# Kernel optimization log

Hardware: AMD Instinct MI355X
Metric: run time of the kernel (lower is better)

The kernel has to match this reference:

```python
import jax, jax.numpy as jnp
import numpy as np

# irreps layout: 256x0e (dim 256) + 128x1o (dim 384) + 64x2e (dim 320) -> total 960
MULS = (256, 128, 64)
DIMS = (1, 3, 5)  # 2l+1 for l = 0, 1, 2


def setup_inputs() -> dict:
    key = jax.random.key(0)
    k0, k1, k2, k3 = jax.random.split(key, 4)
    N = 131072
    total = sum(m * d for m, d in zip(MULS, DIMS))  # 960
    return {
        "features": jax.random.normal(k0, (N, total), dtype=jnp.float32),
        "w0": jax.random.normal(k1, (256, 256), dtype=jnp.float32),
        "w1": jax.random.normal(k2, (128, 128), dtype=jnp.float32),
        "w2": jax.random.normal(k3, (64, 64), dtype=jnp.float32),
    }


def _linear_irreps(features, weights):
    # Equivariant Linear == block-diagonal per-irrep matmul over the multiplicity
    # axis, broadcast over the (2l+1) m-components, scaled by 1/sqrt(mul_in)
    # (the net of e3nn's path_weight sqrt((2l+1)/mul_in) and the w3j 1/sqrt(2l+1)).
    outs = []
    off = 0
    for w, mul, d in zip(weights, MULS, DIMS):
        x = features[:, off:off + mul * d].reshape(-1, mul, d)  # [N, u, i]
        scale = 1.0 / np.sqrt(mul).astype(np.float32)
        y = jnp.einsum('zui,uw->zwi', x, w) * scale  # [N, w, i]
        outs.append(y.reshape(y.shape[0], mul * d))
        off += mul * d
    return jnp.concatenate(outs, axis=-1)  # [N, 960]


def reference(features, w0, w1, w2):
    return _linear_irreps(features, (w0, w1, w2))
```

## Files before the change

### kernel.cpp

```cpp
#include <hip/hip_runtime.h>

typedef short bf16x8 __attribute__((ext_vector_type(8)));
typedef float f32x4 __attribute__((ext_vector_type(4)));

__device__ __forceinline__ unsigned short f2bf(float f) {
    union { float f; unsigned u; } a; a.f = f;
    unsigned u = a.u;
    u += 0x7fffu + ((u >> 16) & 1u);
    return (unsigned short)(u >> 16);
}

__device__ __forceinline__ f32x4 mfma16(bf16x8 a, bf16x8 b, f32x4 c) {
    return __builtin_amdgcn_mfma_f32_16x16x32_bf16(a, b, c, 0, 0, 0);
}

template<int D, int MUL>
__global__ void expand_w(const float* __restrict__ w, unsigned short* __restrict__ wt,
                         float scale) {
    const int n = blockIdx.x;
    const int k = threadIdx.x;
    float v = 0.0f;
    if (D == 1 || (n % D) == (k % D))
        v = w[(k / D) * MUL + (n / D)] * scale;
    wt[n * (MUL * D) + k] = f2bf(v);
}

template<int KP, int OFF, int BASE, bool TAIL>
__device__ __forceinline__ void do_block(const float* __restrict__ xr,
                                         const unsigned short* __restrict__ wb,
                                         float* __restrict__ orow,
                                         unsigned short* As,
                                         int tid, int wv, int lr, int q) {
    constexpr int P     = KP + 8;
    constexpr int KS    = KP / 32;
    constexpr int C8    = KP / 8;
    constexpr int ITERS = KP / 64;
    constexpr int NTW   = TAIL ? 3 : BASE;

    #pragma unroll
    for (int it = 0; it < ITERS; ++it) {
        int idx = tid + it * 512;
        int zl  = idx / C8;
        int c8  = (idx - zl * C8) * 8;
        const float* p = xr + zl * 960 + OFF + c8;
        f32x4 v0 = *(const f32x4*)p;
        f32x4 v1 = *(const f32x4*)(p + 4);
        bf16x8 sv;
        sv[0] = f2bf(v0[0]); sv[1] = f2bf(v0[1]); sv[2] = f2bf(v0[2]); sv[3] = f2bf(v0[3]);
        sv[4] = f2bf(v1[0]); sv[5] = f2bf(v1[1]); sv[6] = f2bf(v1[2]); sv[7] = f2bf(v1[3]);
        *(bf16x8*)(As + zl * P + c8) = sv;
    }
    __syncthreads();

    int nts[NTW];
    #pragma unroll
    for (int in = 0; in < NTW; ++in)
        nts[in] = (!TAIL || in < 2) ? (wv * BASE + in) : (16 + wv);
    const bool t3 = !TAIL || (wv < 4);

    f32x4 acc[4][NTW];
    #pragma unroll
    for (int mt = 0; mt < 4; ++mt)
        #pragma unroll
        for (int in = 0; in < NTW; ++in)
            acc[mt][in] = (f32x4){0.f, 0.f, 0.f, 0.f};

    #pragma unroll
    for (int ks = 0; ks < KS; ++ks) {
        const int kb = ks * 32 + q * 8;
        bf16x8 b[NTW];
        #pragma unroll
        for (int in = 0; in < NTW; ++in)
            if (in < 2 || t3)
                b[in] = *(const bf16x8*)(wb + (nts[in] * 16 + lr) * KP + kb);
        #pragma unroll
        for (int mt = 0; mt < 4; ++mt) {
            bf16x8 a = *(const bf16x8*)(As + (mt * 16 + lr) * P + kb);
            #pragma unroll
            for (int in = 0; in < NTW; ++in)
                if (in < 2 || t3)
                    acc[mt][in] = mfma16(a, b[in], acc[mt][in]);
        }
    }

    #pragma unroll
    for (int mt = 0; mt < 4; ++mt)
        #pragma unroll
        for (int in = 0; in < NTW; ++in)
            if (in < 2 || t3) {
                const int col = OFF + nts[in] * 16 + lr;
                #pragma unroll
                for (int j = 0; j < 4; ++j)
                    orow[(mt * 16 + q * 4 + j) * 960 + col] = acc[mt][in][j];
            }
}

__global__ __launch_bounds__(512, 4)
void fused_linear(const float* __restrict__ x, const unsigned short* __restrict__ wt,
                  float* __restrict__ out) {
    __shared__ __align__(16) unsigned short As[64 * 392];
    const int tid  = threadIdx.x;
    const int lane = tid & 63;
    const int wv   = tid >> 6;
    const int lr   = lane & 15;
    const int q    = lane >> 4;
    const long z0  = (long)blockIdx.x * 64;
    const float* xr = x + z0 * 960;
    float* orow = out + z0 * 960;

    do_block<256,   0, 2, false>(xr, wt,          orow, As, tid, wv, lr, q);
    __syncthreads();
    do_block<384, 256, 3, false>(xr, wt +  65536, orow, As, tid, wv, lr, q);
    __syncthreads();
    do_block<320, 640, 2, true >(xr, wt + 212992, orow, As, tid, wv, lr, q);
}

extern "C" void kernel_launch(void* const* d_in, const int* in_sizes, int n_in,
                              void* d_out, int out_size, void* d_ws, size_t ws_size,
                              hipStream_t stream) {
    const float* x  = (const float*)d_in[0];
    const float* w0 = (const float*)d_in[1];
    const float* w1 = (const float*)d_in[2];
    const float* w2 = (const float*)d_in[3];
    float* out = (float*)d_out;
    unsigned short* wt = (unsigned short*)d_ws;

    const int N = in_sizes[0] / 960;

    expand_w<1, 256><<<256, 256, 0, stream>>>(w0, wt,          0.0625f);
    expand_w<3, 128><<<384, 384, 0, stream>>>(w1, wt +  65536, 0.08838834764831845f);
    expand_w<5,  64><<<320, 320, 0, stream>>>(w2, wt + 212992, 0.125f);

    fused_linear<<<N / 64, 512, 0, stream>>>(x, wt, out);
}
```

Before: 325.8 us.

## Hold activation tiles in registers per wave and drop LDS staging

```diff
diff --git a/kernel.cpp b/kernel.cpp
--- a/kernel.cpp
+++ b/kernel.cpp
@@ -8,6 +8,13 @@
     unsigned u = a.u;
     u += 0x7fffu + ((u >> 16) & 1u);
     return (unsigned short)(u >> 16);
+}
+
+__device__ __forceinline__ bf16x8 pack8(f32x4 v0, f32x4 v1) {
+    bf16x8 r;
+    r[0] = f2bf(v0[0]); r[1] = f2bf(v0[1]); r[2] = f2bf(v0[2]); r[3] = f2bf(v0[3]);
+    r[4] = f2bf(v1[0]); r[5] = f2bf(v1[1]); r[6] = f2bf(v1[2]); r[7] = f2bf(v1[3]);
+    return r;
 }
 
 __device__ __forceinline__ f32x4 mfma16(bf16x8 a, bf16x8 b, f32x4 c) {
@@ -25,94 +32,70 @@
     wt[n * (MUL * D) + k] = f2bf(v);
 }
 
-template<int KP, int OFF, int BASE, bool TAIL>
-__device__ __forceinline__ void do_block(const float* __restrict__ xr,
+template<int KP, int OFF, int MT>
+__device__ __forceinline__ void do_block(const float* __restrict__ xw,
                                          const unsigned short* __restrict__ wb,
-                                         float* __restrict__ orow,
-                                         unsigned short* As,
-                                         int tid, int wv, int lr, int q) {
-    constexpr int P     = KP + 8;
-    constexpr int KS    = KP / 32;
-    constexpr int C8    = KP / 8;
-    constexpr int ITERS = KP / 64;
-    constexpr int NTW   = TAIL ? 3 : BASE;
+                                         float* __restrict__ ow,
+                                         int lr, int q) {
+    constexpr int KS = KP / 32;
 
+    bf16x8 a[MT][KS];
     #pragma unroll
-    for (int it = 0; it < ITERS; ++it) {
-        int idx = tid + it * 512;
-        int zl  = idx / C8;
-        int c8  = (idx - zl * C8) * 8;
-        const float* p = xr + zl * 960 + OFF + c8;
-        f32x4 v0 = *(const f32x4*)p;
-        f32x4 v1 = *(const f32x4*)(p + 4);
-        bf16x8 sv;
-        sv[0] = f2bf(v0[0]); sv[1] = f2bf(v0[1]); sv[2] = f2bf(v0[2]); sv[3] = f2bf(v0[3]);
-        sv[4] = f2bf(v1[0]); sv[5] = f2bf(v1[1]); sv[6] = f2bf(v1[2]); sv[7] = f2bf(v1[3]);
-        *(bf16x8*)(As + zl * P + c8) = sv;
+    for (int mt = 0; mt < MT; ++mt)
+        #pragma unroll
+        for (int ks = 0; ks < KS; ++ks) {
+            const float* p = xw + mt * (16 * 960) + OFF + ks * 32;
+            a[mt][ks] = pack8(*(const f32x4*)p, *(const f32x4*)(p + 4));
+        }
+
+    const unsigned short* bp = wb + lr * KP + q * 8;
+    #pragma unroll 1
+    for (int c = 0; c < KS; ++c) {
+        const unsigned short* b0p = bp + (c * 32 + 0)  * KP;
+        const unsigned short* b1p = bp + (c * 32 + 16) * KP;
+        f32x4 acc[MT][2];
+        #pragma unroll
+        for (int mt = 0; mt < MT; ++mt) {
+            acc[mt][0] = (f32x4){0.f, 0.f, 0.f, 0.f};
+            acc[mt][1] = (f32x4){0.f, 0.f, 0.f, 0.f};
+        }
+        #pragma unroll
+        for (int ks = 0; ks < KS; ++ks) {
+            bf16x8 b0 = *(const bf16x8*)(b0p + ks * 32);
+            bf16x8 b1 = *(const bf16x8*)(b1p + ks * 32);
+            #pragma unroll
+            for (int mt = 0; mt < MT; ++mt) {
+                acc[mt][0] = mfma16(a[mt][ks], b0, acc[mt][0]);
+                acc[mt][1] = mfma16(a[mt][ks], b1, acc[mt][1]);
+            }
+        }
+        #pragma unroll
+        for (int mt = 0; mt < MT; ++mt)
+            #pragma unroll
+            for (int j = 0; j < 4; ++j) {
+                float* po = ow + (mt * 16 + j) * 960 + OFF + c * 32;
+                po[0]  = acc[mt][0][j];
+                po[16] = acc[mt][1][j];
+            }
     }
-    __syncthreads();
-
-    int nts[NTW];
-    #pragma unroll
-    for (int in = 0; in < NTW; ++in)
-        nts[in] = (!TAIL || in < 2) ? (wv * BASE + in) : (16 + wv);
-    const bool t3 = !TAIL || (wv < 4);
-
-    f32x4 acc[4][NTW];
-    #pragma unroll
-    for (int mt = 0; mt < 4; ++mt)
-        #pragma unroll
-        for (int in = 0; in < NTW; ++in)
-            acc[mt][in] = (f32x4){0.f, 0.f, 0.f, 0.f};
-
-    #pragma unroll
-    for (int ks = 0; ks < KS; ++ks) {
-        const int kb = ks * 32 + q * 8;
-        bf16x8 b[NTW];
-        #pragma unroll
-        for (int in = 0; in < NTW; ++in)
-            if (in < 2 || t3)
-                b[in] = *(const bf16x8*)(wb + (nts[in] * 16 + lr) * KP + kb);
-        #pragma unroll
-        for (int mt = 0; mt < 4; ++mt) {
-            bf16x8 a = *(const bf16x8*)(As + (mt * 16 + lr) * P + kb);
-            #pragma unroll
-            for (int in = 0; in < NTW; ++in)
-                if (in < 2 || t3)
-                    acc[mt][in] = mfma16(a, b[in], acc[mt][in]);
-        }
-    }
-
-    #pragma unroll
-    for (int mt = 0; mt < 4; ++mt)
-        #pragma unroll
-        for (int in = 0; in < NTW; ++in)
-            if (in < 2 || t3) {
-                const int col = OFF + nts[in] * 16 + lr;
-                #pragma unroll
-                for (int j = 0; j < 4; ++j)
-                    orow[(mt * 16 + q * 4 + j) * 960 + col] = acc[mt][in][j];
-            }
 }
 
-__global__ __launch_bounds__(512, 4)
+__global__ __launch_bounds__(256)
 void fused_linear(const float* __restrict__ x, const unsigned short* __restrict__ wt,
                   float* __restrict__ out) {
-    __shared__ __align__(16) unsigned short As[64 * 392];
     const int tid  = threadIdx.x;
     const int lane = tid & 63;
-    const int wv   = tid >> 6;
     const int lr   = lane & 15;
     const int q    = lane >> 4;
-    const long z0  = (long)blockIdx.x * 64;
-    const float* xr = x + z0 * 960;
-    float* orow = out + z0 * 960;
+    const long z0  = ((long)blockIdx.x * 4 + (tid >> 6)) * 32;
 
-    do_block<256,   0, 2, false>(xr, wt,          orow, As, tid, wv, lr, q);
-    __syncthreads();
-    do_block<384, 256, 3, false>(xr, wt +  65536, orow, As, tid, wv, lr, q);
-    __syncthreads();
-    do_block<320, 640, 2, true >(xr, wt + 212992, orow, As, tid, wv, lr, q);
+    const float* xw = x   + (z0 + lr) * 960 + q * 8;
+    float*       ow = out + (z0 + q * 4) * 960 + lr;
+
+    do_block<256,   0, 2>(xw, wt,          ow, lr, q);
+    do_block<384, 256, 1>(xw,            wt + 65536, ow,            lr, q);
+    do_block<384, 256, 1>(xw + 16 * 960, wt + 65536, ow + 16 * 960, lr, q);
+    do_block<320, 640, 2>(xw, wt + 212992, ow, lr, q);
 }
 
 extern "C" void kernel_launch(void* const* d_in, const int* in_sizes, int n_in,
@@ -131,5 +114,5 @@
     expand_w<3, 128><<<384, 384, 0, stream>>>(w1, wt +  65536, 0.08838834764831845f);
     expand_w<5,  64><<<320, 320, 0, stream>>>(w2, wt + 212992, 0.125f);
 
-    fused_linear<<<N / 64, 512, 0, stream>>>(x, wt, out);
+    fused_linear<<<N / 128, 256, 0, stream>>>(x, wt, out);
 }
```

After: 537.5 us. 1.65x slower.

## Split irrep blocks across separate workgroups with swizzled LDS and 4-wave blocks

Applied to the files above, without the earlier changes.

```diff
diff --git a/kernel.cpp b/kernel.cpp
--- a/kernel.cpp
+++ b/kernel.cpp
@@ -1,13 +1,12 @@
 #include <hip/hip_runtime.h>
+#include <hip/hip_bf16.h>
 
 typedef short bf16x8 __attribute__((ext_vector_type(8)));
 typedef float f32x4 __attribute__((ext_vector_type(4)));
+typedef unsigned short u16t;
 
-__device__ __forceinline__ unsigned short f2bf(float f) {
-    union { float f; unsigned u; } a; a.f = f;
-    unsigned u = a.u;
-    u += 0x7fffu + ((u >> 16) & 1u);
-    return (unsigned short)(u >> 16);
+__device__ __forceinline__ u16t f2bf(float f) {
+    return __builtin_bit_cast(u16t, __float2bfloat16(f));
 }
 
 __device__ __forceinline__ f32x4 mfma16(bf16x8 a, bf16x8 b, f32x4 c) {
@@ -15,8 +14,7 @@
 }
 
 template<int D, int MUL>
-__global__ void expand_w(const float* __restrict__ w, unsigned short* __restrict__ wt,
-                         float scale) {
+__global__ void expand_w(const float* __restrict__ w, u16t* __restrict__ wt, float scale) {
     const int n = blockIdx.x;
     const int k = threadIdx.x;
     float v = 0.0f;
@@ -25,94 +23,80 @@
     wt[n * (MUL * D) + k] = f2bf(v);
 }
 
-template<int KP, int OFF, int BASE, bool TAIL>
-__device__ __forceinline__ void do_block(const float* __restrict__ xr,
-                                         const unsigned short* __restrict__ wb,
-                                         float* __restrict__ orow,
-                                         unsigned short* As,
-                                         int tid, int wv, int lr, int q) {
-    constexpr int P     = KP + 8;
-    constexpr int KS    = KP / 32;
-    constexpr int C8    = KP / 8;
-    constexpr int ITERS = KP / 64;
-    constexpr int NTW   = TAIL ? 3 : BASE;
+template<int KP, int NTH>
+__device__ __forceinline__ void compute_half(const char* __restrict__ arow,
+                                             const u16t* __restrict__ wb,
+                                             float* __restrict__ orow,
+                                             int nt0, int lr, int q) {
+    constexpr int KS = KP / 32;
+    f32x4 acc[4][NTH] = {};
+    #pragma unroll
+    for (int ks = 0; ks < KS; ++ks) {
+        bf16x8 b[NTH];
+        #pragma unroll
+        for (int nt = 0; nt < NTH; ++nt)
+            b[nt] = *(const bf16x8*)(wb + ((nt0 + nt) * 16 + lr) * KP + ks * 32 + q * 8);
+        #pragma unroll
+        for (int mt = 0; mt < 4; ++mt) {
+            bf16x8 a = *(const bf16x8*)(arow + mt * 16 * KP * 2 +
+                                        ((ks * 64 + q * 16) ^ ((lr & 7) << 4)));
+            #pragma unroll
+            for (int nt = 0; nt < NTH; ++nt)
+                acc[mt][nt] = mfma16(a, b[nt], acc[mt][nt]);
+        }
+    }
+    #pragma unroll
+    for (int mt = 0; mt < 4; ++mt)
+        #pragma unroll
+        for (int nt = 0; nt < NTH; ++nt)
+            #pragma unroll
+            for (int j = 0; j < 4; ++j)
+                orow[(mt * 16 + q * 4 + j) * 960 + (nt0 + nt) * 16 + lr] = acc[mt][nt][j];
+}
+
+template<int KP, int OFF, int NTH0, int NTH1>
+__device__ __forceinline__ void do_block(const float* __restrict__ x,
+                                         const u16t* __restrict__ wb,
+                                         float* __restrict__ out,
+                                         char* smem, long tile, int tid) {
+    constexpr int C8  = KP / 8;
+    constexpr int NCH = 64 * C8 / 256;
+    constexpr int NTW = NTH0 + NTH1;
+    const int lane = tid & 63, wv = tid >> 6, lr = lane & 15, q = lane >> 4;
+    const float* xr = x + tile * 64 * 960 + OFF;
+    float* orow = out + tile * 64 * 960 + OFF;
 
     #pragma unroll
-    for (int it = 0; it < ITERS; ++it) {
-        int idx = tid + it * 512;
-        int zl  = idx / C8;
-        int c8  = (idx - zl * C8) * 8;
-        const float* p = xr + zl * 960 + OFF + c8;
+    for (int it = 0; it < NCH; ++it) {
+        int idx = tid + it * 256;
+        int row = idx / C8;
+        int c8  = idx % C8;
+        const float* p = xr + row * 960 + c8 * 8;
         f32x4 v0 = *(const f32x4*)p;
         f32x4 v1 = *(const f32x4*)(p + 4);
         bf16x8 sv;
         sv[0] = f2bf(v0[0]); sv[1] = f2bf(v0[1]); sv[2] = f2bf(v0[2]); sv[3] = f2bf(v0[3]);
         sv[4] = f2bf(v1[0]); sv[5] = f2bf(v1[1]); sv[6] = f2bf(v1[2]); sv[7] = f2bf(v1[3]);
-        *(bf16x8*)(As + zl * P + c8) = sv;
+        *(bf16x8*)(smem + row * (KP * 2) + ((c8 * 16) ^ ((row & 7) << 4))) = sv;
     }
     __syncthreads();
 
-    int nts[NTW];
-    #pragma unroll
-    for (int in = 0; in < NTW; ++in)
-        nts[in] = (!TAIL || in < 2) ? (wv * BASE + in) : (16 + wv);
-    const bool t3 = !TAIL || (wv < 4);
-
-    f32x4 acc[4][NTW];
-    #pragma unroll
-    for (int mt = 0; mt < 4; ++mt)
-        #pragma unroll
-        for (int in = 0; in < NTW; ++in)
-            acc[mt][in] = (f32x4){0.f, 0.f, 0.f, 0.f};
-
-    #pragma unroll
-    for (int ks = 0; ks < KS; ++ks) {
-        const int kb = ks * 32 + q * 8;
-        bf16x8 b[NTW];
-        #pragma unroll
-        for (int in = 0; in < NTW; ++in)
-            if (in < 2 || t3)
-                b[in] = *(const bf16x8*)(wb + (nts[in] * 16 + lr) * KP + kb);
-        #pragma unroll
-        for (int mt = 0; mt < 4; ++mt) {
-            bf16x8 a = *(const bf16x8*)(As + (mt * 16 + lr) * P + kb);
-            #pragma unroll
-            for (int in = 0; in < NTW; ++in)
-                if (in < 2 || t3)
-                    acc[mt][in] = mfma16(a, b[in], acc[mt][in]);
-        }
-    }
-
-    #pragma unroll
-    for (int mt = 0; mt < 4; ++mt)
-        #pragma unroll
-        for (int in = 0; in < NTW; ++in)
-            if (in < 2 || t3) {
-                const int col = OFF + nts[in] * 16 + lr;
-                #pragma unroll
-                for (int j = 0; j < 4; ++j)
-                    orow[(mt * 16 + q * 4 + j) * 960 + col] = acc[mt][in][j];
-            }
+    const char* arow = smem + lr * (KP * 2);
+    compute_half<KP, NTH0>(arow, wb, orow, wv * NTW,        lr, q);
+    compute_half<KP, NTH1>(arow, wb, orow, wv * NTW + NTH0, lr, q);
 }
 
-__global__ __launch_bounds__(512, 4)
-void fused_linear(const float* __restrict__ x, const unsigned short* __restrict__ wt,
+__global__ __launch_bounds__(256, 3)
+void fused_linear(const float* __restrict__ x, const u16t* __restrict__ wt,
                   float* __restrict__ out) {
-    __shared__ __align__(16) unsigned short As[64 * 392];
-    const int tid  = threadIdx.x;
-    const int lane = tid & 63;
-    const int wv   = tid >> 6;
-    const int lr   = lane & 15;
-    const int q    = lane >> 4;
-    const long z0  = (long)blockIdx.x * 64;
-    const float* xr = x + z0 * 960;
-    float* orow = out + z0 * 960;
-
-    do_block<256,   0, 2, false>(xr, wt,          orow, As, tid, wv, lr, q);
-    __syncthreads();
-    do_block<384, 256, 3, false>(xr, wt +  65536, orow, As, tid, wv, lr, q);
-    __syncthreads();
-    do_block<320, 640, 2, true >(xr, wt + 212992, orow, As, tid, wv, lr, q);
+    __shared__ __align__(16) char smem[64 * 384 * 2];
+    const long gid  = blockIdx.x;
+    const int  bt   = (int)(gid % 3);
+    const long tile = gid / 3;
+    const int  tid  = threadIdx.x;
+    if (bt == 0)      do_block<256,   0, 2, 2>(x, wt,          out, smem, tile, tid);
+    else if (bt == 1) do_block<384, 256, 3, 3>(x, wt +  65536, out, smem, tile, tid);
+    else              do_block<320, 640, 3, 2>(x, wt + 212992, out, smem, tile, tid);
 }
 
 extern "C" void kernel_launch(void* const* d_in, const int* in_sizes, int n_in,
@@ -123,13 +107,14 @@
     const float* w1 = (const float*)d_in[2];
     const float* w2 = (const float*)d_in[3];
     float* out = (float*)d_out;
-    unsigned short* wt = (unsigned short*)d_ws;
+    u16t* wt = (u16t*)d_ws;
 
-    const int N = in_sizes[0] / 960;
+    const int N     = in_sizes[0] / 960;
+    const int tiles = N / 64;
 
     expand_w<1, 256><<<256, 256, 0, stream>>>(w0, wt,          0.0625f);
     expand_w<3, 128><<<384, 384, 0, stream>>>(w1, wt +  65536, 0.08838834764831845f);
     expand_w<5,  64><<<320, 320, 0, stream>>>(w2, wt + 212992, 0.125f);
 
-    fused_linear<<<N / 64, 512, 0, stream>>>(x, wt, out);
+    fused_linear<<<3 * tiles, 256, 0, stream>>>(x, wt, out);
 }
```

Result: slower. 338.4 us (+3.9%).
